# Kernel optimization log

Hardware: AMD Instinct MI355X
Metric: run time of the kernel (lower is better)

## Reference

```python
import jax, jax.numpy as jnp
import numpy as np

D_MODEL = 1024
NUM_HEADS = 16
D_K = D_MODEL // NUM_HEADS


def setup_inputs() -> dict:
    key = jax.random.key(0)
    ks = jax.random.split(key, 11)
    B, S, D = 4, 2048, D_MODEL
    scale = 1.0 / np.sqrt(D)
    inp = {
        'query': jax.random.normal(ks[0], (B, S, D), jnp.float32),
        'key':   jax.random.normal(ks[1], (B, S, D), jnp.float32),
        'value': jax.random.normal(ks[2], (B, S, D), jnp.float32),
        'Wq': jax.random.normal(ks[3], (D, D), jnp.float32) * scale,
        'bq': jnp.zeros((D,), jnp.float32),
        'Wk': jax.random.normal(ks[4], (D, D), jnp.float32) * scale,
        'bk': jnp.zeros((D,), jnp.float32),
        'Wv': jax.random.normal(ks[5], (D, D), jnp.float32) * scale,
        'bv': jnp.zeros((D,), jnp.float32),
        'Wo': jax.random.normal(ks[6], (D, D), jnp.float32) * scale,
        'bo': jnp.zeros((D,), jnp.float32),
    }
    return inp


def _mha(query, key, value, Wq, bq, Wk, bk, Wv, bv, Wo, bo):
    B, S, D = query.shape
    H, dk = NUM_HEADS, D_K
    # Linear projections then split heads: [B, S, D] -> [B, H, S, dk]
    def split_heads(x):
        return x.reshape(B, S, H, dk).transpose(0, 2, 1, 3)
    Q = split_heads(query @ Wq + bq)
    K = split_heads(key @ Wk + bk)
    V = split_heads(value @ Wv + bv)
    # Scores: [B, H, S, S]
    scores = jnp.einsum('bhqd,bhkd->bhqk', Q, K) / jnp.sqrt(jnp.float32(dk)).astype(Q.dtype)
    attn = jax.nn.softmax(scores, axis=-1)
    # Context: [B, H, S, dk] -> [B, S, D]
    ctx = jnp.einsum('bhqk,bhkd->bhqd', attn, V)
    ctx = ctx.transpose(0, 2, 1, 3).reshape(B, S, D)
    return ctx @ Wo + bo


def reference(query, key, value, Wq, bq, Wk, bk, Wv, bv, Wo, bo):
    return _mha(query, key, value, Wq, bq, Wk, bk, Wv, bv, Wo, bo)
```

## Files before the change

### kernel.cpp

```cpp
#include <hip/hip_runtime.h>

typedef __attribute__((ext_vector_type(8))) short s8v;
typedef __attribute__((ext_vector_type(4))) float f4v;

#define MFMA16(a, b, c) __builtin_amdgcn_mfma_f32_16x16x32_bf16(a, b, c, 0, 0, 0)

__device__ __forceinline__ unsigned short f2bf(float f) {
    union { float f; unsigned int u; } v; v.f = f;
    unsigned int u = v.u;
    unsigned int r = (u + 0x7FFFu + ((u >> 16) & 1u)) >> 16;
    return (unsigned short)r;
}

__device__ __forceinline__ unsigned int cvt_pk_bf16(float lo, float hi) {
    unsigned int r;
    asm volatile("v_cvt_pk_bf16_f32 %0, %1, %2" : "=v"(r) : "v"(lo), "v"(hi));
    return r;
}

__global__ __launch_bounds__(256) void transpose_cvt_k(
        const float* __restrict__ W0, const float* __restrict__ W1,
        const float* __restrict__ W2, const float* __restrict__ W3,
        unsigned short* __restrict__ T0, unsigned short* __restrict__ T1,
        unsigned short* __restrict__ T2, unsigned short* __restrict__ T3) {
    __shared__ float tile[32][33];
    const float* W; unsigned short* T;
    switch (blockIdx.z) {
        case 0:  W = W0; T = T0; break;
        case 1:  W = W1; T = T1; break;
        case 2:  W = W2; T = T2; break;
        default: W = W3; T = T3; break;
    }
    int tx = threadIdx.x & 31, ty = threadIdx.x >> 5;
    int k0 = blockIdx.x * 32, n0 = blockIdx.y * 32;
#pragma unroll
    for (int i = 0; i < 32; i += 8)
        tile[ty + i][tx] = W[(size_t)(k0 + ty + i) * 1024 + n0 + tx];
    __syncthreads();
#pragma unroll
    for (int i = 0; i < 32; i += 8)
        T[(size_t)(n0 + ty + i) * 1024 + k0 + tx] = f2bf(tile[tx][ty + i]);
}

template <typename AT, int OUT_MODE>
__global__ __launch_bounds__(256, 2) void gemm_bt_k(
        const AT* __restrict__ A, const unsigned short* __restrict__ Bt,
        const float* __restrict__ bias, void* __restrict__ C) {
    constexpr int Kd = 1024, Nd = 1024;
    constexpr int BK = 64;
    constexpr int LDT = 72;
    __shared__ __attribute__((aligned(16))) unsigned short As[128 * LDT];
    __shared__ __attribute__((aligned(16))) unsigned short Bs[128 * LDT];

    const int tid  = threadIdx.x;
    const int lane = tid & 63, wave = tid >> 6;
    const int g = lane >> 4, li = lane & 15;
    const int wr = wave >> 1, wc = wave & 1;
    const int row0 = blockIdx.y * 128, col0 = blockIdx.x * 128;

    f4v acc[4][4];
#pragma unroll
    for (int m = 0; m < 4; m++)
#pragma unroll
        for (int n = 0; n < 4; n++) acc[m][n] = (f4v){0.f, 0.f, 0.f, 0.f};

    for (int kt = 0; kt < Kd; kt += BK) {
        __syncthreads();
#pragma unroll
        for (int i = 0; i < 4; i++) {
            int e = (i * 256 + tid) * 8;
            int r = e >> 6, kk = e & 63;
            s8v a8;
            if constexpr (sizeof(AT) == 4) {
                const float* ap = (const float*)A + (size_t)(row0 + r) * Kd + kt + kk;
                float4 x = *reinterpret_cast<const float4*>(ap);
                float4 y = *reinterpret_cast<const float4*>(ap + 4);
                a8[0] = (short)f2bf(x.x); a8[1] = (short)f2bf(x.y);
                a8[2] = (short)f2bf(x.z); a8[3] = (short)f2bf(x.w);
                a8[4] = (short)f2bf(y.x); a8[5] = (short)f2bf(y.y);
                a8[6] = (short)f2bf(y.z); a8[7] = (short)f2bf(y.w);
            } else {
                a8 = *reinterpret_cast<const s8v*>(
                        (const unsigned short*)A + (size_t)(row0 + r) * Kd + kt + kk);
            }
            *reinterpret_cast<s8v*>(&As[r * LDT + kk]) = a8;
            s8v b8 = *reinterpret_cast<const s8v*>(Bt + (size_t)(col0 + r) * Kd + kt + kk);
            *reinterpret_cast<s8v*>(&Bs[r * LDT + kk]) = b8;
        }
        __syncthreads();

        s8v af[4][2], bf[4][2];
#pragma unroll
        for (int m = 0; m < 4; m++)
#pragma unroll
            for (int ks = 0; ks < 2; ks++)
                af[m][ks] = *reinterpret_cast<const s8v*>(
                        &As[(wr * 64 + m * 16 + li) * LDT + ks * 32 + g * 8]);
#pragma unroll
        for (int n = 0; n < 4; n++)
#pragma unroll
            for (int ks = 0; ks < 2; ks++)
                bf[n][ks] = *reinterpret_cast<const s8v*>(
                        &Bs[(wc * 64 + n * 16 + li) * LDT + ks * 32 + g * 8]);
#pragma unroll
        for (int ks = 0; ks < 2; ks++)
#pragma unroll
            for (int m = 0; m < 4; m++)
#pragma unroll
                for (int n = 0; n < 4; n++)
                    acc[m][n] = MFMA16(af[m][ks], bf[n][ks], acc[m][n]);
    }

#pragma unroll
    for (int n = 0; n < 4; n++) {
        int col = col0 + wc * 64 + n * 16 + li;
        float bv = bias[col];
#pragma unroll
        for (int m = 0; m < 4; m++) {
            int rbase = row0 + wr * 64 + m * 16 + g * 4;
            if constexpr (OUT_MODE == 2) {
                int h = col >> 6, d = col & 63;
                int b = rbase >> 11, s = rbase & 2047;
                ushort4 pk;
                pk.x = f2bf(acc[m][n][0] + bv);
                pk.y = f2bf(acc[m][n][1] + bv);
                pk.z = f2bf(acc[m][n][2] + bv);
                pk.w = f2bf(acc[m][n][3] + bv);
                *reinterpret_cast<ushort4*>(
                    (unsigned short*)C + ((((size_t)b * 16 + h) * 64 + d) * 2048 + s)) = pk;
            } else {
#pragma unroll
                for (int r = 0; r < 4; r++) {
                    float v = acc[m][n][r] + bv;
                    if constexpr (OUT_MODE == 1)
                        ((float*)C)[(size_t)(rbase + r) * Nd + col] = v;
                    else
                        ((unsigned short*)C)[(size_t)(rbase + r) * Nd + col] = f2bf(v);
                }
            }
        }
    }
}

__global__ __launch_bounds__(256, 2) void attn_k(
        const unsigned short* __restrict__ Q, const unsigned short* __restrict__ K,
        const unsigned short* __restrict__ Vt, unsigned short* __restrict__ Ctx) {
    constexpr int S = 2048, Dm = 1024, DKh = 64;
    constexpr int LDK = 72, LDV = 136, LDP = 40;
    constexpr float CEXP = 0.125f * 1.44269504f;
    __shared__ __attribute__((aligned(16))) unsigned short K_lds[128 * LDK];
    __shared__ __attribute__((aligned(16))) unsigned short V_lds[64 * LDV];
    __shared__ __attribute__((aligned(16))) unsigned short P_lds[4][32 * LDP];

    const int tid  = threadIdx.x;
    const int lane = tid & 63, wave = tid >> 6;
    const int g = lane >> 4, li = lane & 15;
    const int id = blockIdx.x;
    const int bh = (id & 7) * 8 + ((id >> 3) & 7);
    const int qp = id >> 6;
    const int b = bh >> 4, h = bh & 15;
    const size_t base  = (size_t)b * S * Dm + (size_t)h * DKh;
    const size_t vbase = (size_t)bh * DKh * S;
    const int q00 = qp * 256 + wave * 32;

    s8v qf[2][2][2];
#pragma unroll
    for (int qt = 0; qt < 2; qt++)
#pragma unroll
        for (int rb = 0; rb < 2; rb++)
#pragma unroll
            for (int ks = 0; ks < 2; ks++)
                qf[qt][rb][ks] = *reinterpret_cast<const s8v*>(
                        Q + base + (size_t)(q00 + qt * 128 + rb * 16 + li) * Dm
                           + ks * 32 + g * 8);

    f4v octx[2][2][4];
    float m_run[2][2][4], l_run[2][2][4];
#pragma unroll
    for (int qt = 0; qt < 2; qt++)
#pragma unroll
        for (int rb = 0; rb < 2; rb++) {
#pragma unroll
            for (int nb = 0; nb < 4; nb++) octx[qt][rb][nb] = (f4v){0.f, 0.f, 0.f, 0.f};
#pragma unroll
            for (int r = 0; r < 4; r++) { m_run[qt][rb][r] = -1e30f; l_run[qt][rb][r] = 0.f; }
        }

    const int rdswz = ((li >> 2) & 3) << 3;

    for (int t = 0; t < 16; t++) {
        const int kv0 = t * 128;
        __syncthreads();
#pragma unroll
        for (int i = 0; i < 4; i++) {
            int e = (i * 256 + tid) * 8;
            int s = e >> 6, d = e & 63;
            *reinterpret_cast<s8v*>(&K_lds[s * LDK + d]) =
                *reinterpret_cast<const s8v*>(K + base + (size_t)(kv0 + s) * Dm + d);
            int dv = e >> 7, sv = e & 127;
            *reinterpret_cast<s8v*>(&V_lds[dv * LDV + sv]) =
                *reinterpret_cast<const s8v*>(Vt + vbase + (size_t)dv * S + kv0 + sv);
        }
        __syncthreads();

#pragma unroll
        for (int qt = 0; qt < 2; qt++) {
            f4v sc[2][8];
#pragma unroll
            for (int rb = 0; rb < 2; rb++)
#pragma unroll
                for (int cb = 0; cb < 8; cb++) sc[rb][cb] = (f4v){0.f, 0.f, 0.f, 0.f};
#pragma unroll
            for (int cb = 0; cb < 8; cb++) {
#pragma unroll
                for (int ks = 0; ks < 2; ks++) {
                    s8v kf = *reinterpret_cast<const s8v*>(
                            &K_lds[(cb * 16 + li) * LDK + ks * 32 + g * 8]);
                    sc[0][cb] = MFMA16(qf[qt][0][ks], kf, sc[0][cb]);
                    sc[1][cb] = MFMA16(qf[qt][1][ks], kf, sc[1][cb]);
                }
            }

            float rsum[2][4];
#pragma unroll
            for (int rb = 0; rb < 2; rb++) {
                float rmax[4];
#pragma unroll
                for (int r = 0; r < 4; r++) {
                    float v = sc[rb][0][r];
#pragma unroll
                    for (int cb = 1; cb < 8; cb++) v = fmaxf(v, sc[rb][cb][r]);
                    rmax[r] = v * CEXP;
                }
#pragma unroll
                for (int mask = 1; mask < 16; mask <<= 1)
#pragma unroll
                    for (int r = 0; r < 4; r++)
                        rmax[r] = fmaxf(rmax[r], __shfl_xor(rmax[r], mask, 64));
#pragma unroll
                for (int r = 0; r < 4; r++) {
                    float mn = fmaxf(m_run[qt][rb][r], rmax[r]);
                    float scl = __builtin_amdgcn_exp2f(m_run[qt][rb][r] - mn);
                    m_run[qt][rb][r] = mn;
                    l_run[qt][rb][r] *= scl;
                    rsum[rb][r] = 0.f;
#pragma unroll
                    for (int nb = 0; nb < 4; nb++) octx[qt][rb][nb][r] *= scl;
                }
            }

#pragma unroll
            for (int ks = 0; ks < 4; ks++) {
#pragma unroll
                for (int rb = 0; rb < 2; rb++) {
#pragma unroll
                    for (int cc = 0; cc < 2; cc++) {
                        int cb = ks * 2 + cc;
                        float p0 = __builtin_amdgcn_exp2f(fmaf(sc[rb][cb][0], CEXP, -m_run[qt][rb][0]));
                        float p1 = __builtin_amdgcn_exp2f(fmaf(sc[rb][cb][1], CEXP, -m_run[qt][rb][1]));
                        float p2 = __builtin_amdgcn_exp2f(fmaf(sc[rb][cb][2], CEXP, -m_run[qt][rb][2]));
                        float p3 = __builtin_amdgcn_exp2f(fmaf(sc[rb][cb][3], CEXP, -m_run[qt][rb][3]));
                        rsum[rb][0] += p0; rsum[rb][1] += p1;
                        rsum[rb][2] += p2; rsum[rb][3] += p3;
                        unsigned int u01 = cvt_pk_bf16(p0, p1);
                        unsigned int u23 = cvt_pk_bf16(p2, p3);
                        int rowb = rb * 16 + g * 4;
                        int colS = (cc * 16 + li) ^ (g << 3);
                        P_lds[wave][(rowb + 0) * LDP + colS] = (unsigned short)u01;
                        P_lds[wave][(rowb + 1) * LDP + colS] = (unsigned short)(u01 >> 16);
                        P_lds[wave][(rowb + 2) * LDP + colS] = (unsigned short)u23;
                        P_lds[wave][(rowb + 3) * LDP + colS] = (unsigned short)(u23 >> 16);
                    }
                }
                s8v vf[4], pf[2];
#pragma unroll
                for (int nb = 0; nb < 4; nb++)
                    vf[nb] = *reinterpret_cast<const s8v*>(
                            &V_lds[(nb * 16 + li) * LDV + ks * 32 + g * 8]);
#pragma unroll
                for (int rb = 0; rb < 2; rb++)
                    pf[rb] = *reinterpret_cast<const s8v*>(
                            &P_lds[wave][(rb * 16 + li) * LDP + ((g * 8) ^ rdswz)]);
#pragma unroll
                for (int rb = 0; rb < 2; rb++)
#pragma unroll
                    for (int nb = 0; nb < 4; nb++)
                        octx[qt][rb][nb] = MFMA16(pf[rb], vf[nb], octx[qt][rb][nb]);
            }

#pragma unroll
            for (int mask = 1; mask < 16; mask <<= 1)
#pragma unroll
                for (int rb = 0; rb < 2; rb++)
#pragma unroll
                    for (int r = 0; r < 4; r++)
                        rsum[rb][r] += __shfl_xor(rsum[rb][r], mask, 64);
#pragma unroll
            for (int rb = 0; rb < 2; rb++)
#pragma unroll
                for (int r = 0; r < 4; r++) l_run[qt][rb][r] += rsum[rb][r];
        }
    }

#pragma unroll
    for (int qt = 0; qt < 2; qt++)
#pragma unroll
        for (int rb = 0; rb < 2; rb++)
#pragma unroll
            for (int r = 0; r < 4; r++) {
                float inv = 1.0f / l_run[qt][rb][r];
                int row = q00 + qt * 128 + rb * 16 + g * 4 + r;
#pragma unroll
                for (int nb = 0; nb < 4; nb++) {
                    int d = nb * 16 + li;
                    Ctx[base + (size_t)row * Dm + d] = f2bf(octx[qt][rb][nb][r] * inv);
                }
            }
}

extern "C" void kernel_launch(void* const* d_in, const int* in_sizes, int n_in,
                              void* d_out, int out_size, void* d_ws, size_t ws_size,
                              hipStream_t stream) {
    const float* query = (const float*)d_in[0];
    const float* key   = (const float*)d_in[1];
    const float* value = (const float*)d_in[2];
    const float* Wq = (const float*)d_in[3];
    const float* bq = (const float*)d_in[4];
    const float* Wk = (const float*)d_in[5];
    const float* bk = (const float*)d_in[6];
    const float* Wv = (const float*)d_in[7];
    const float* bv = (const float*)d_in[8];
    const float* Wo = (const float*)d_in[9];
    const float* bo = (const float*)d_in[10];

    unsigned short* ws = (unsigned short*)d_ws;
    const size_t MD = (size_t)8192 * 1024;
    unsigned short* Qb  = ws;
    unsigned short* Kb  = Qb + MD;
    unsigned short* Vtb = Kb + MD;
    unsigned short* Cb  = Vtb + MD;
    unsigned short* Wqt = Cb + MD;
    unsigned short* Wkt = Wqt + 1024 * 1024;
    unsigned short* Wvt = Wkt + 1024 * 1024;
    unsigned short* Wot = Wvt + 1024 * 1024;

    transpose_cvt_k<<<dim3(32, 32, 4), 256, 0, stream>>>(Wq, Wk, Wv, Wo, Wqt, Wkt, Wvt, Wot);
    gemm_bt_k<float, 0><<<dim3(8, 64), 256, 0, stream>>>(query, Wqt, bq, Qb);
    gemm_bt_k<float, 0><<<dim3(8, 64), 256, 0, stream>>>(key,   Wkt, bk, Kb);
    gemm_bt_k<float, 2><<<dim3(8, 64), 256, 0, stream>>>(value, Wvt, bv, Vtb);
    attn_k<<<512, 256, 0, stream>>>(Qb, Kb, Vtb, Cb);
    gemm_bt_k<unsigned short, 1><<<dim3(8, 64), 256, 0, stream>>>(Cb, Wot, bo, (float*)d_out);
}
```

Measured before the change: 331.2 us.

## Pre-convert activations to bf16 and load GEMM tiles via global_load_lds

```diff
diff --git a/kernel.cpp b/kernel.cpp
--- a/kernel.cpp
+++ b/kernel.cpp
@@ -16,6 +16,34 @@
     unsigned int r;
     asm volatile("v_cvt_pk_bf16_f32 %0, %1, %2" : "=v"(r) : "v"(lo), "v"(hi));
     return r;
+}
+
+__device__ __forceinline__ void gl16(const void* g, void* l) {
+    __builtin_amdgcn_global_load_lds(
+        (const __attribute__((address_space(1))) void*)g,
+        (__attribute__((address_space(3))) void*)l, 16, 0, 0);
+}
+
+__global__ __launch_bounds__(256) void cvt_bf16_k(
+        const float* __restrict__ X0, const float* __restrict__ X1,
+        const float* __restrict__ X2,
+        unsigned short* __restrict__ Y0, unsigned short* __restrict__ Y1,
+        unsigned short* __restrict__ Y2) {
+    const float* X; unsigned short* Y;
+    switch (blockIdx.y) {
+        case 0:  X = X0; Y = Y0; break;
+        case 1:  X = X1; Y = Y1; break;
+        default: X = X2; Y = Y2; break;
+    }
+    size_t i = ((size_t)blockIdx.x * 256 + threadIdx.x) * 8;
+    float4 a = *reinterpret_cast<const float4*>(X + i);
+    float4 b = *reinterpret_cast<const float4*>(X + i + 4);
+    s8v o;
+    o[0] = (short)f2bf(a.x); o[1] = (short)f2bf(a.y);
+    o[2] = (short)f2bf(a.z); o[3] = (short)f2bf(a.w);
+    o[4] = (short)f2bf(b.x); o[5] = (short)f2bf(b.y);
+    o[6] = (short)f2bf(b.z); o[7] = (short)f2bf(b.w);
+    *reinterpret_cast<s8v*>(Y + i) = o;
 }
 
 __global__ __launch_bounds__(256) void transpose_cvt_k(
@@ -42,21 +70,20 @@
         T[(size_t)(n0 + ty + i) * 1024 + k0 + tx] = f2bf(tile[tx][ty + i]);
 }
 
-template <typename AT, int OUT_MODE>
+template <int OUT_MODE>
 __global__ __launch_bounds__(256, 2) void gemm_bt_k(
-        const AT* __restrict__ A, const unsigned short* __restrict__ Bt,
+        const unsigned short* __restrict__ A, const unsigned short* __restrict__ Bt,
         const float* __restrict__ bias, void* __restrict__ C) {
     constexpr int Kd = 1024, Nd = 1024;
-    constexpr int BK = 64;
-    constexpr int LDT = 72;
-    __shared__ __attribute__((aligned(16))) unsigned short As[128 * LDT];
-    __shared__ __attribute__((aligned(16))) unsigned short Bs[128 * LDT];
+    __shared__ __attribute__((aligned(16))) unsigned short As[128 * 32];
+    __shared__ __attribute__((aligned(16))) unsigned short Bs[128 * 32];
 
     const int tid  = threadIdx.x;
     const int lane = tid & 63, wave = tid >> 6;
     const int g = lane >> 4, li = lane & 15;
     const int wr = wave >> 1, wc = wave & 1;
     const int row0 = blockIdx.y * 128, col0 = blockIdx.x * 128;
+    const int lrow = lane >> 2, lcol = (lane & 3) * 8;
 
     f4v acc[4][4];
 #pragma unroll
@@ -64,51 +91,30 @@
 #pragma unroll
         for (int n = 0; n < 4; n++) acc[m][n] = (f4v){0.f, 0.f, 0.f, 0.f};
 
-    for (int kt = 0; kt < Kd; kt += BK) {
+    for (int kt = 0; kt < Kd; kt += 32) {
         __syncthreads();
 #pragma unroll
-        for (int i = 0; i < 4; i++) {
-            int e = (i * 256 + tid) * 8;
-            int r = e >> 6, kk = e & 63;
-            s8v a8;
-            if constexpr (sizeof(AT) == 4) {
-                const float* ap = (const float*)A + (size_t)(row0 + r) * Kd + kt + kk;
-                float4 x = *reinterpret_cast<const float4*>(ap);
-                float4 y = *reinterpret_cast<const float4*>(ap + 4);
-                a8[0] = (short)f2bf(x.x); a8[1] = (short)f2bf(x.y);
-                a8[2] = (short)f2bf(x.z); a8[3] = (short)f2bf(x.w);
-                a8[4] = (short)f2bf(y.x); a8[5] = (short)f2bf(y.y);
-                a8[6] = (short)f2bf(y.z); a8[7] = (short)f2bf(y.w);
-            } else {
-                a8 = *reinterpret_cast<const s8v*>(
-                        (const unsigned short*)A + (size_t)(row0 + r) * Kd + kt + kk);
-            }
-            *reinterpret_cast<s8v*>(&As[r * LDT + kk]) = a8;
-            s8v b8 = *reinterpret_cast<const s8v*>(Bt + (size_t)(col0 + r) * Kd + kt + kk);
-            *reinterpret_cast<s8v*>(&Bs[r * LDT + kk]) = b8;
+        for (int jj = 0; jj < 2; jj++) {
+            int j = wave * 2 + jj;
+            gl16(A  + (size_t)(row0 + j * 16 + lrow) * Kd + kt + lcol, &As[j * 512]);
+            gl16(Bt + (size_t)(col0 + j * 16 + lrow) * Kd + kt + lcol, &Bs[j * 512]);
         }
         __syncthreads();
 
-        s8v af[4][2], bf[4][2];
+        s8v af[4], bf[4];
 #pragma unroll
         for (int m = 0; m < 4; m++)
-#pragma unroll
-            for (int ks = 0; ks < 2; ks++)
-                af[m][ks] = *reinterpret_cast<const s8v*>(
-                        &As[(wr * 64 + m * 16 + li) * LDT + ks * 32 + g * 8]);
+            af[m] = *reinterpret_cast<const s8v*>(&As[(wr * 64 + m * 16 + li) * 32 + g * 8]);
 #pragma unroll
         for (int n = 0; n < 4; n++)
-#pragma unroll
-            for (int ks = 0; ks < 2; ks++)
-                bf[n][ks] = *reinterpret_cast<const s8v*>(
-                        &Bs[(wc * 64 + n * 16 + li) * LDT + ks * 32 + g * 8]);
-#pragma unroll
-        for (int ks = 0; ks < 2; ks++)
-#pragma unroll
-            for (int m = 0; m < 4; m++)
-#pragma unroll
-                for (int n = 0; n < 4; n++)
-                    acc[m][n] = MFMA16(af[m][ks], bf[n][ks], acc[m][n]);
+            bf[n] = *reinterpret_cast<const s8v*>(&Bs[(wc * 64 + n * 16 + li) * 32 + g * 8]);
+        __builtin_amdgcn_s_setprio(1);
+#pragma unroll
+        for (int m = 0; m < 4; m++)
+#pragma unroll
+            for (int n = 0; n < 4; n++)
+                acc[m][n] = MFMA16(af[m], bf[n], acc[m][n]);
+        __builtin_amdgcn_s_setprio(0);
     }
 
 #pragma unroll
@@ -210,6 +216,7 @@
             for (int rb = 0; rb < 2; rb++)
 #pragma unroll
                 for (int cb = 0; cb < 8; cb++) sc[rb][cb] = (f4v){0.f, 0.f, 0.f, 0.f};
+            __builtin_amdgcn_s_setprio(1);
 #pragma unroll
             for (int cb = 0; cb < 8; cb++) {
 #pragma unroll
@@ -220,6 +227,7 @@
                     sc[1][cb] = MFMA16(qf[qt][1][ks], kf, sc[1][cb]);
                 }
             }
+            __builtin_amdgcn_s_setprio(0);
 
             float rsum[2][4];
 #pragma unroll
@@ -281,11 +289,13 @@
                 for (int rb = 0; rb < 2; rb++)
                     pf[rb] = *reinterpret_cast<const s8v*>(
                             &P_lds[wave][(rb * 16 + li) * LDP + ((g * 8) ^ rdswz)]);
+                __builtin_amdgcn_s_setprio(1);
 #pragma unroll
                 for (int rb = 0; rb < 2; rb++)
 #pragma unroll
                     for (int nb = 0; nb < 4; nb++)
                         octx[qt][rb][nb] = MFMA16(pf[rb], vf[nb], octx[qt][rb][nb]);
+                __builtin_amdgcn_s_setprio(0);
             }
 
 #pragma unroll
@@ -339,15 +349,19 @@
     unsigned short* Kb  = Qb + MD;
     unsigned short* Vtb = Kb + MD;
     unsigned short* Cb  = Vtb + MD;
-    unsigned short* Wqt = Cb + MD;
+    unsigned short* Qx  = Cb + MD;
+    unsigned short* Kx  = Qx + MD;
+    unsigned short* Vx  = Kx + MD;
+    unsigned short* Wqt = Vx + MD;
     unsigned short* Wkt = Wqt + 1024 * 1024;
     unsigned short* Wvt = Wkt + 1024 * 1024;
     unsigned short* Wot = Wvt + 1024 * 1024;
 
+    cvt_bf16_k<<<dim3(4096, 3), 256, 0, stream>>>(query, key, value, Qx, Kx, Vx);
     transpose_cvt_k<<<dim3(32, 32, 4), 256, 0, stream>>>(Wq, Wk, Wv, Wo, Wqt, Wkt, Wvt, Wot);
-    gemm_bt_k<float, 0><<<dim3(8, 64), 256, 0, stream>>>(query, Wqt, bq, Qb);
-    gemm_bt_k<float, 0><<<dim3(8, 64), 256, 0, stream>>>(key,   Wkt, bk, Kb);
-    gemm_bt_k<float, 2><<<dim3(8, 64), 256, 0, stream>>>(value, Wvt, bv, Vtb);
+    gemm_bt_k<0><<<dim3(8, 64), 256, 0, stream>>>(Qx, Wqt, bq, Qb);
+    gemm_bt_k<0><<<dim3(8, 64), 256, 0, stream>>>(Kx, Wkt, bk, Kb);
+    gemm_bt_k<2><<<dim3(8, 64), 256, 0, stream>>>(Vx, Wvt, bv, Vtb);
     attn_k<<<512, 256, 0, stream>>>(Qb, Kb, Vtb, Cb);
-    gemm_bt_k<unsigned short, 1><<<dim3(8, 64), 256, 0, stream>>>(Cb, Wot, bo, (float*)d_out);
-}
+    gemm_bt_k<1><<<dim3(8, 64), 256, 0, stream>>>(Cb, Wot, bo, (float*)d_out);
+}
```

Result: faster. 300.3 us (-9.3%).
